# Optimization experiments

Hardware: AMD Instinct MI355X
Metric: run time of the kernel (lower is better)

## Reference

```python
import jax, jax.numpy as jnp
import numpy as np


def setup_inputs() -> dict:
    key = jax.random.key(0)
    ks = jax.random.split(key, 7)
    B, S, D, HD, m = 4, 8192, 2048, 128, 4
    s = 0.02
    return {
        "h": jax.random.normal(ks[0], (B, S, D), jnp.float32),
        "w_kv_a": jax.random.normal(ks[1], (D, HD), jnp.float32) * s,
        "w_kv_b": jax.random.normal(ks[2], (D, HD), jnp.float32) * s,
        "w_z_a": jax.random.normal(ks[3], (D, HD), jnp.float32) * s,
        "w_z_b": jax.random.normal(ks[4], (D, HD), jnp.float32) * s,
        "b_a": jax.random.normal(ks[5], (m, HD), jnp.float32) * s,
        "b_b": jax.random.normal(ks[6], (m, HD), jnp.float32) * s,
        "m": m,
    }


def reference(h, w_kv_a, w_kv_b, w_z_a, w_z_b, b_a, b_b, m):
    # h: [B, S, D]; weights stored as [D, head_dim] (torch Linear W^T)
    B, S, D = h.shape
    HD = w_kv_a.shape[1]
    n = S // m  # number of compressed blocks
    # Projections, reshaped into m-token blocks: [B, n, m, HD]
    c_a = (h @ w_kv_a).reshape(B, n, m, HD)
    c_b = (h @ w_kv_b).reshape(B, n, m, HD)
    z_a = (h @ w_z_a).reshape(B, n, m, HD)
    z_b = (h @ w_z_b).reshape(B, n, m, HD)

    def prev(x):  # previous block per position (block 0 has no predecessor)
        return jnp.concatenate([jnp.zeros_like(x[:, :1]), x[:, :-1]], axis=1)

    # Window of 2m logits per block: [prev-block b-branch, current-block a-branch]
    logits = jnp.concatenate([prev(z_b) + b_b, z_a + b_a], axis=2)  # [B, n, 2m, HD]
    # Block 0 only sees its own m tokens: mask out the (absent) previous half
    valid = jnp.concatenate(
        [jnp.broadcast_to((jnp.arange(n) > 0)[:, None], (n, m)),
         jnp.ones((n, m), bool)], axis=1)  # [n, 2m]
    neg = jnp.finfo(logits.dtype).min
    logits = jnp.where(valid[None, :, :, None], logits, neg)
    weights = jax.nn.softmax(logits, axis=2)  # softmax over the 2m window, per feature
    c_vals = jnp.concatenate([prev(c_b), c_a], axis=2)  # [B, n, 2m, HD]
    compressed = jnp.sum(weights * c_vals, axis=2)  # [B, n, HD]
    return compressed, compressed
```

## Files before the change

### kernel.cpp

```cpp
#include <hip/hip_runtime.h>

typedef unsigned short u16;
typedef unsigned int u32;
typedef float f32x4 __attribute__((ext_vector_type(4)));
typedef short bf16x8 __attribute__((ext_vector_type(8)));
typedef u16 u16x8 __attribute__((ext_vector_type(8)));

#define D_DIM 2048
#define HD_DIM 128
#define NCOLS 512
#define BM 128
#define HALO 16
#define MROWS 144
#define BK 32
#define KSTEPS 64
#define NTHREADS 512
#define OUT1 1048576

#define A_STRIDE 40
#define A_BYTES (MROWS * A_STRIDE * 2)
#define B_BYTES (NCOLS * BK * 2)
#define OFF_A0 0
#define OFF_A1 A_BYTES
#define OFF_B0 (2 * A_BYTES)
#define OFF_B1 (OFF_B0 + B_BYTES)
#define EPI_STRIDE 520
#define SMEM_BYTES (MROWS * EPI_STRIDE * 2)

__device__ __forceinline__ u16 f2bf(float f) {
  u32 u = __builtin_bit_cast(u32, f);
  u32 r = u + 0x7FFFu + ((u >> 16) & 1u);
  return (u16)(r >> 16);
}
__device__ __forceinline__ float bf2f(u16 v) {
  u32 u = ((u32)v) << 16;
  return __builtin_bit_cast(float, u);
}

__global__ __launch_bounds__(256) void wconv_kernel(
    const float* __restrict__ w0, const float* __restrict__ w1,
    const float* __restrict__ w2, const float* __restrict__ w3,
    u16* __restrict__ Wt) {
  __shared__ float tile[64][129];
  const int t = threadIdx.x;
  const int mat = blockIdx.x >> 5;
  const int k0 = (blockIdx.x & 31) << 6;
  const float* w = (mat == 0) ? w0 : (mat == 1) ? w1 : (mat == 2) ? w2 : w3;
#pragma unroll
  for (int i = 0; i < 32; ++i) {
    int idx = t + i * 256;
    int r = idx >> 7, c = idx & 127;
    tile[r][c] = w[(k0 + r) * HD_DIM + c];
  }
  __syncthreads();
#pragma unroll
  for (int i = 0; i < 32; ++i) {
    int idx = t + i * 256;
    int nl = idx >> 6, kk = idx & 63;
    Wt[(long)(mat * HD_DIM + nl) * D_DIM + k0 + kk] = f2bf(tile[kk][nl]);
  }
}

__global__ __launch_bounds__(NTHREADS, 2) void fused_kernel(
    const float* __restrict__ h, const u16* __restrict__ Wt,
    const float* __restrict__ ba, const float* __restrict__ bb,
    float* __restrict__ out) {
  __shared__ alignas(16) unsigned char smem[SMEM_BYTES];
  const int t = threadIdx.x;
  const int w = t >> 6;
  const int l = t & 63;
  const int r0 = blockIdx.x * BM;

  const int arow0 = t >> 2;
  const int aseg0 = t & 3;
  const int ag0 = r0 - HALO + arow0;
  const bool av0 = (ag0 >= 0);
  const float* asrc0 = h + (long)ag0 * D_DIM + aseg0 * 8;
  const int adst0 = arow0 * A_STRIDE + aseg0 * 8;

  const bool has2 = ((t & 7) == 0);
  const int q2 = 512 + (t >> 3);
  const int arow1 = q2 >> 2;
  const int aseg1 = q2 & 3;
  const float* asrc1 = h + (long)(r0 - HALO + arow1) * D_DIM + aseg1 * 8;
  const int adst1 = arow1 * A_STRIDE + aseg1 * 8;

  const int brow = t >> 2;
  const int bc = t & 3;
  const int bswz = bc ^ ((t >> 3) & 3);
  const u16* bsrc0 = Wt + (long)brow * D_DIM + bc * 8;
  const int bdst = brow * 32 + bswz * 8;

  const int aoff0 = (l & 15) * A_STRIDE + (l >> 4) * 8;
  const int swzr = (l >> 4) ^ ((l >> 1) & 3);
  const int boff0 = (w * 64 + (l & 15)) * 32 + swzr * 8;

  f32x4 acc[9][4];
#pragma unroll
  for (int mt = 0; mt < 9; ++mt)
#pragma unroll
    for (int nt = 0; nt < 4; ++nt) acc[mt][nt] = (f32x4){0.f, 0.f, 0.f, 0.f};

  float4 la0a, la0b, la1a, la1b;
  u16x8 bs0, bs1, bs2, bs3;

#define DO_LOADS(K0)                                          \
  {                                                           \
    const float4 z4 = make_float4(0.f, 0.f, 0.f, 0.f);        \
    la0a = av0 ? *(const float4*)(asrc0 + (K0)) : z4;         \
    la0b = av0 ? *(const float4*)(asrc0 + (K0) + 4) : z4;     \
    if (has2) {                                               \
      la1a = *(const float4*)(asrc1 + (K0));                  \
      la1b = *(const float4*)(asrc1 + (K0) + 4);              \
    }                                                         \
    bs0 = *(const u16x8*)(bsrc0 + (K0));                      \
    bs1 = *(const u16x8*)(bsrc0 + 128 * 2048 + (K0));         \
    bs2 = *(const u16x8*)(bsrc0 + 256 * 2048 + (K0));         \
    bs3 = *(const u16x8*)(bsrc0 + 384 * 2048 + (K0));         \
  }

#define DO_STORE(BUF)                                         \
  {                                                           \
    u16* Ab = (u16*)(smem + ((BUF) ? OFF_A1 : OFF_A0));       \
    u16* Bb = (u16*)(smem + ((BUF) ? OFF_B1 : OFF_B0));       \
    u16x8 pa;                                                 \
    pa[0] = f2bf(la0a.x); pa[1] = f2bf(la0a.y);               \
    pa[2] = f2bf(la0a.z); pa[3] = f2bf(la0a.w);               \
    pa[4] = f2bf(la0b.x); pa[5] = f2bf(la0b.y);               \
    pa[6] = f2bf(la0b.z); pa[7] = f2bf(la0b.w);               \
    *(u16x8*)(Ab + adst0) = pa;                               \
    if (has2) {                                               \
      u16x8 pb;                                               \
      pb[0] = f2bf(la1a.x); pb[1] = f2bf(la1a.y);             \
      pb[2] = f2bf(la1a.z); pb[3] = f2bf(la1a.w);             \
      pb[4] = f2bf(la1b.x); pb[5] = f2bf(la1b.y);             \
      pb[6] = f2bf(la1b.z); pb[7] = f2bf(la1b.w);             \
      *(u16x8*)(Ab + adst1) = pb;                             \
    }                                                         \
    *(u16x8*)(Bb + bdst) = bs0;                               \
    *(u16x8*)(Bb + 128 * 32 + bdst) = bs1;                    \
    *(u16x8*)(Bb + 256 * 32 + bdst) = bs2;                    \
    *(u16x8*)(Bb + 384 * 32 + bdst) = bs3;                    \
  }

  DO_LOADS(0)
  DO_STORE(0)
  __syncthreads();

  for (int step = 0; step < KSTEPS; ++step) {
    const int cur = step & 1;
    const bool more = (step + 1) < KSTEPS;
    if (more) DO_LOADS((step + 1) * BK)
    {
      const u16* Ab = (const u16*)(smem + (cur ? OFF_A1 : OFF_A0));
      const u16* Bb = (const u16*)(smem + (cur ? OFF_B1 : OFF_B0));
      bf16x8 bfr[4];
#pragma unroll
      for (int nt = 0; nt < 4; ++nt)
        bfr[nt] = *(const bf16x8*)(Bb + boff0 + nt * (16 * 32));
#pragma unroll
      for (int mt = 0; mt < 9; ++mt) {
        bf16x8 af = *(const bf16x8*)(Ab + aoff0 + mt * (16 * A_STRIDE));
#pragma unroll
        for (int nt = 0; nt < 4; ++nt)
          acc[mt][nt] = __builtin_amdgcn_mfma_f32_16x16x32_bf16(
              af, bfr[nt], acc[mt][nt], 0, 0, 0);
      }
    }
    if (more) DO_STORE(cur ^ 1)
    __syncthreads();
  }

  u16* E = (u16*)smem;
  {
    const int er = (l >> 4) * 4;
    const int ec = w * 64 + (l & 15);
#pragma unroll
    for (int mt = 0; mt < 9; ++mt)
#pragma unroll
      for (int nt = 0; nt < 4; ++nt)
#pragma unroll
        for (int j = 0; j < 4; ++j)
          E[(mt * 16 + er + j) * EPI_STRIDE + ec + nt * 16] =
              f2bf(acc[mt][nt][j]);
  }
  __syncthreads();

  {
    const int hd = t & 127;
    const int grp = t >> 7;
    const int b = r0 >> 13;
    const int sbase = r0 & 8191;
#pragma unroll
    for (int i = 0; i < 8; ++i) {
      const int nblk = grp * 8 + i;
      const int s_in = sbase + nblk * 4;
      const bool first = (s_in == 0);
      const int rc = HALO + nblk * 4;
      float la[4], lb[4], ca[4], cb[4];
#pragma unroll
      for (int j = 0; j < 4; ++j) {
        const u16* rowc = E + (rc + j) * EPI_STRIDE;
        const u16* rowp = E + (rc - 4 + j) * EPI_STRIDE;
        la[j] = bf2f(rowc[256 + hd]) + ba[j * 128 + hd];
        ca[j] = bf2f(rowc[hd]);
        lb[j] = first ? -3.0e38f
                      : (bf2f(rowp[384 + hd]) + bb[j * 128 + hd]);
        cb[j] = bf2f(rowp[128 + hd]);
      }
      float mx = la[0];
#pragma unroll
      for (int j = 1; j < 4; ++j) mx = fmaxf(mx, la[j]);
#pragma unroll
      for (int j = 0; j < 4; ++j) mx = fmaxf(mx, lb[j]);
      float num = 0.f, den = 0.f;
#pragma unroll
      for (int j = 0; j < 4; ++j) {
        float ea = __expf(la[j] - mx);
        num += ea * ca[j]; den += ea;
        float eb = __expf(lb[j] - mx);
        num += eb * cb[j]; den += eb;
      }
      const float res = num / den;
      const int o = ((b << 11) + (s_in >> 2)) * HD_DIM + hd;
      out[o] = res;
      out[o + OUT1] = res;
    }
  }
}

extern "C" void kernel_launch(void* const* d_in, const int* in_sizes, int n_in,
                              void* d_out, int out_size, void* d_ws,
                              size_t ws_size, hipStream_t stream) {
  (void)in_sizes; (void)n_in; (void)out_size; (void)ws_size;
  const float* h = (const float*)d_in[0];
  const float* w_kv_a = (const float*)d_in[1];
  const float* w_kv_b = (const float*)d_in[2];
  const float* w_z_a = (const float*)d_in[3];
  const float* w_z_b = (const float*)d_in[4];
  const float* b_a = (const float*)d_in[5];
  const float* b_b = (const float*)d_in[6];
  u16* Wt = (u16*)d_ws;
  float* out = (float*)d_out;
  wconv_kernel<<<128, 256, 0, stream>>>(w_kv_a, w_kv_b, w_z_a, w_z_b, Wt);
  fused_kernel<<<256, NTHREADS, 0, stream>>>(h, Wt, b_a, b_b, out);
}
```

Measured before the change: 496.5 us.

## Triple-buffer K loop with direct global-to-LDS weight loads and pre-swizzled weights

Pre-swizzles the bf16 weight matrix in the conversion kernel into per-K-step tiles in LDS order, so the main kernel can copy them straight from global memory into LDS with global_load_lds and skip the register round trip. The activation tile stays register-staged but is now prefetched two steps ahead, with a three-buffer LDS rotation, manual vmcnt waits and a single barrier per step. The goal is to hide global load latency behind MFMA work and cut VGPR and LDS-store instruction pressure. The cost is more complex hand-written waitcnt logic, a tighter LDS budget, and some correctness risk in the buffer indexing.

```diff
diff --git a/kernel.cpp b/kernel.cpp
--- a/kernel.cpp
+++ b/kernel.cpp
@@ -8,7 +8,6 @@
 
 #define D_DIM 2048
 #define HD_DIM 128
-#define NCOLS 512
 #define BM 128
 #define HALO 16
 #define MROWS 144
@@ -19,11 +18,8 @@
 
 #define A_STRIDE 40
 #define A_BYTES (MROWS * A_STRIDE * 2)
-#define B_BYTES (NCOLS * BK * 2)
-#define OFF_A0 0
-#define OFF_A1 A_BYTES
-#define OFF_B0 (2 * A_BYTES)
-#define OFF_B1 (OFF_B0 + B_BYTES)
+#define B_BYTES (512 * BK * 2)
+#define OFF_A (3 * B_BYTES)
 #define EPI_STRIDE 520
 #define SMEM_BYTES (MROWS * EPI_STRIDE * 2)
 
@@ -35,6 +31,12 @@
 __device__ __forceinline__ float bf2f(u16 v) {
   u32 u = ((u32)v) << 16;
   return __builtin_bit_cast(float, u);
+}
+
+__device__ __forceinline__ void gload_lds16(const u16* g, u16* l) {
+  __builtin_amdgcn_global_load_lds(
+      (const __attribute__((address_space(1))) unsigned int*)g,
+      (__attribute__((address_space(3))) unsigned int*)l, 16, 0, 0);
 }
 
 __global__ __launch_bounds__(256) void wconv_kernel(
@@ -57,7 +59,11 @@
   for (int i = 0; i < 32; ++i) {
     int idx = t + i * 256;
     int nl = idx >> 6, kk = idx & 63;
-    Wt[(long)(mat * HD_DIM + nl) * D_DIM + k0 + kk] = f2bf(tile[kk][nl]);
+    int n = mat * HD_DIM + nl;
+    int k = k0 + kk;
+    int stepi = k >> 5, kr = k & 31;
+    int pos = stepi * 16384 + n * 32 + (((kr >> 3) ^ ((n >> 1) & 3)) << 3) + (kr & 7);
+    Wt[pos] = f2bf(tile[kk][nl]);
   }
 }
 
@@ -71,25 +77,17 @@
   const int l = t & 63;
   const int r0 = blockIdx.x * BM;
 
-  const int arow0 = t >> 2;
-  const int aseg0 = t & 3;
+  const int arow0 = t >> 2, aseg0 = t & 3;
   const int ag0 = r0 - HALO + arow0;
   const bool av0 = (ag0 >= 0);
-  const float* asrc0 = h + (long)ag0 * D_DIM + aseg0 * 8;
+  const long ag0c = av0 ? (long)ag0 : 0l;
+  const float* asrc0 = h + ag0c * D_DIM + aseg0 * 8;
   const int adst0 = arow0 * A_STRIDE + aseg0 * 8;
-
   const bool has2 = ((t & 7) == 0);
-  const int q2 = 512 + (t >> 3);
-  const int arow1 = q2 >> 2;
-  const int aseg1 = q2 & 3;
+  const int arow1 = 128 + (t >> 5);
+  const int aseg1 = (t >> 3) & 3;
   const float* asrc1 = h + (long)(r0 - HALO + arow1) * D_DIM + aseg1 * 8;
   const int adst1 = arow1 * A_STRIDE + aseg1 * 8;
-
-  const int brow = t >> 2;
-  const int bc = t & 3;
-  const int bswz = bc ^ ((t >> 3) & 3);
-  const u16* bsrc0 = Wt + (long)brow * D_DIM + bc * 8;
-  const int bdst = brow * 32 + bswz * 8;
 
   const int aoff0 = (l & 15) * A_STRIDE + (l >> 4) * 8;
   const int swzr = (l >> 4) ^ ((l >> 1) & 3);
@@ -101,75 +99,108 @@
 #pragma unroll
     for (int nt = 0; nt < 4; ++nt) acc[mt][nt] = (f32x4){0.f, 0.f, 0.f, 0.f};
 
-  float4 la0a, la0b, la1a, la1b;
-  u16x8 bs0, bs1, bs2, bs3;
-
-#define DO_LOADS(K0)                                          \
-  {                                                           \
-    const float4 z4 = make_float4(0.f, 0.f, 0.f, 0.f);        \
-    la0a = av0 ? *(const float4*)(asrc0 + (K0)) : z4;         \
-    la0b = av0 ? *(const float4*)(asrc0 + (K0) + 4) : z4;     \
-    if (has2) {                                               \
-      la1a = *(const float4*)(asrc1 + (K0));                  \
-      la1b = *(const float4*)(asrc1 + (K0) + 4);              \
-    }                                                         \
-    bs0 = *(const u16x8*)(bsrc0 + (K0));                      \
-    bs1 = *(const u16x8*)(bsrc0 + 128 * 2048 + (K0));         \
-    bs2 = *(const u16x8*)(bsrc0 + 256 * 2048 + (K0));         \
-    bs3 = *(const u16x8*)(bsrc0 + 384 * 2048 + (K0));         \
-  }
-
-#define DO_STORE(BUF)                                         \
-  {                                                           \
-    u16* Ab = (u16*)(smem + ((BUF) ? OFF_A1 : OFF_A0));       \
-    u16* Bb = (u16*)(smem + ((BUF) ? OFF_B1 : OFF_B0));       \
-    u16x8 pa;                                                 \
-    pa[0] = f2bf(la0a.x); pa[1] = f2bf(la0a.y);               \
-    pa[2] = f2bf(la0a.z); pa[3] = f2bf(la0a.w);               \
-    pa[4] = f2bf(la0b.x); pa[5] = f2bf(la0b.y);               \
-    pa[6] = f2bf(la0b.z); pa[7] = f2bf(la0b.w);               \
-    *(u16x8*)(Ab + adst0) = pa;                               \
-    if (has2) {                                               \
-      u16x8 pb;                                               \
-      pb[0] = f2bf(la1a.x); pb[1] = f2bf(la1a.y);             \
-      pb[2] = f2bf(la1a.z); pb[3] = f2bf(la1a.w);             \
-      pb[4] = f2bf(la1b.x); pb[5] = f2bf(la1b.y);             \
-      pb[6] = f2bf(la1b.z); pb[7] = f2bf(la1b.w);             \
-      *(u16x8*)(Ab + adst1) = pb;                             \
-    }                                                         \
-    *(u16x8*)(Bb + bdst) = bs0;                               \
-    *(u16x8*)(Bb + 128 * 32 + bdst) = bs1;                    \
-    *(u16x8*)(Bb + 256 * 32 + bdst) = bs2;                    \
-    *(u16x8*)(Bb + 384 * 32 + bdst) = bs3;                    \
-  }
-
-  DO_LOADS(0)
-  DO_STORE(0)
+  float4 r0a, r0b, r0ha, r0hb, r1a, r1b, r1ha, r1hb;
+
+#define ISSUE_B(SI, BI)                                           \
+  {                                                               \
+    const u16* gsrc = Wt + (size_t)(SI) * 16384 + w * 2048 + l * 8; \
+    u16* lb = (u16*)(smem + (BI) * B_BYTES) + w * 2048;           \
+    gload_lds16(gsrc, lb);                                        \
+    gload_lds16(gsrc + 512, lb + 512);                            \
+    gload_lds16(gsrc + 1024, lb + 1024);                          \
+    gload_lds16(gsrc + 1536, lb + 1536);                          \
+  }
+
+#define ISSUE_A(SI, RA, RB, RHA, RHB)      \
+  {                                        \
+    const float* p0 = asrc0 + (SI) * BK;   \
+    RA = *(const float4*)(p0);             \
+    RB = *(const float4*)(p0 + 4);         \
+    if (has2) {                            \
+      const float* p1 = asrc1 + (SI) * BK; \
+      RHA = *(const float4*)(p1);          \
+      RHB = *(const float4*)(p1 + 4);      \
+    }                                      \
+  }
+
+#define WRITE_A(BI, RA, RB, RHA, RHB)                  \
+  {                                                    \
+    u16* Ab = (u16*)(smem + OFF_A + (BI) * A_BYTES);   \
+    u16x8 pa;                                          \
+    pa[0] = av0 ? f2bf(RA.x) : (u16)0;                 \
+    pa[1] = av0 ? f2bf(RA.y) : (u16)0;                 \
+    pa[2] = av0 ? f2bf(RA.z) : (u16)0;                 \
+    pa[3] = av0 ? f2bf(RA.w) : (u16)0;                 \
+    pa[4] = av0 ? f2bf(RB.x) : (u16)0;                 \
+    pa[5] = av0 ? f2bf(RB.y) : (u16)0;                 \
+    pa[6] = av0 ? f2bf(RB.z) : (u16)0;                 \
+    pa[7] = av0 ? f2bf(RB.w) : (u16)0;                 \
+    *(u16x8*)(Ab + adst0) = pa;                        \
+    if (has2) {                                        \
+      u16x8 pb;                                        \
+      pb[0] = f2bf(RHA.x); pb[1] = f2bf(RHA.y);        \
+      pb[2] = f2bf(RHA.z); pb[3] = f2bf(RHA.w);        \
+      pb[4] = f2bf(RHB.x); pb[5] = f2bf(RHB.y);        \
+      pb[6] = f2bf(RHB.z); pb[7] = f2bf(RHB.w);        \
+      *(u16x8*)(Ab + adst1) = pb;                      \
+    }                                                  \
+  }
+
+#define COMPUTE(BI)                                                         \
+  {                                                                         \
+    const u16* Ab = (const u16*)(smem + OFF_A + (BI) * A_BYTES);            \
+    const u16* Bb = (const u16*)(smem + (BI) * B_BYTES);                    \
+    bf16x8 bfr0 = *(const bf16x8*)(Bb + boff0);                             \
+    bf16x8 bfr1 = *(const bf16x8*)(Bb + boff0 + 512);                       \
+    bf16x8 bfr2 = *(const bf16x8*)(Bb + boff0 + 1024);                      \
+    bf16x8 bfr3 = *(const bf16x8*)(Bb + boff0 + 1536);                      \
+    _Pragma("unroll")                                                       \
+    for (int mt = 0; mt < 9; ++mt) {                                        \
+      bf16x8 af = *(const bf16x8*)(Ab + aoff0 + mt * (16 * A_STRIDE));      \
+      acc[mt][0] = __builtin_amdgcn_mfma_f32_16x16x32_bf16(af, bfr0, acc[mt][0], 0, 0, 0); \
+      acc[mt][1] = __builtin_amdgcn_mfma_f32_16x16x32_bf16(af, bfr1, acc[mt][1], 0, 0, 0); \
+      acc[mt][2] = __builtin_amdgcn_mfma_f32_16x16x32_bf16(af, bfr2, acc[mt][2], 0, 0, 0); \
+      acc[mt][3] = __builtin_amdgcn_mfma_f32_16x16x32_bf16(af, bfr3, acc[mt][3], 0, 0, 0); \
+    }                                                                       \
+  }
+
+#define VM_WAIT8() asm volatile("s_waitcnt vmcnt(8)" ::: "memory")
+#define VM_WAIT0() asm volatile("s_waitcnt vmcnt(0)" ::: "memory")
+#define SYNC_ITER()                                        \
+  {                                                        \
+    asm volatile("s_waitcnt lgkmcnt(0)" ::: "memory");     \
+    __builtin_amdgcn_s_barrier();                          \
+  }
+
+  ISSUE_B(0, 0)
+  ISSUE_A(0, r0a, r0b, r0ha, r0hb)
+  ISSUE_B(1, 1)
+  ISSUE_A(1, r1a, r1b, r1ha, r1hb)
+  VM_WAIT8();
+  WRITE_A(0, r0a, r0b, r0ha, r0hb)
+  SYNC_ITER();
+
+  for (int s = 0; s < KSTEPS - 2; s += 2) {
+    const int b0 = s % 3, b1 = (s + 1) % 3, b2 = (s + 2) % 3, b3 = (s + 3) % 3;
+    ISSUE_B(s + 2, b2)
+    ISSUE_A(s + 2, r0a, r0b, r0ha, r0hb)
+    VM_WAIT8();
+    WRITE_A(b1, r1a, r1b, r1ha, r1hb)
+    COMPUTE(b0)
+    SYNC_ITER();
+    ISSUE_B(s + 3, b3)
+    ISSUE_A(s + 3, r1a, r1b, r1ha, r1hb)
+    VM_WAIT8();
+    WRITE_A(b2, r0a, r0b, r0ha, r0hb)
+    COMPUTE(b1)
+    SYNC_ITER();
+  }
+  VM_WAIT0();
+  WRITE_A(0, r1a, r1b, r1ha, r1hb)
+  COMPUTE(2)
+  SYNC_ITER();
+  COMPUTE(0)
   __syncthreads();
-
-  for (int step = 0; step < KSTEPS; ++step) {
-    const int cur = step & 1;
-    const bool more = (step + 1) < KSTEPS;
-    if (more) DO_LOADS((step + 1) * BK)
-    {
-      const u16* Ab = (const u16*)(smem + (cur ? OFF_A1 : OFF_A0));
-      const u16* Bb = (const u16*)(smem + (cur ? OFF_B1 : OFF_B0));
-      bf16x8 bfr[4];
-#pragma unroll
-      for (int nt = 0; nt < 4; ++nt)
-        bfr[nt] = *(const bf16x8*)(Bb + boff0 + nt * (16 * 32));
-#pragma unroll
-      for (int mt = 0; mt < 9; ++mt) {
-        bf16x8 af = *(const bf16x8*)(Ab + aoff0 + mt * (16 * A_STRIDE));
-#pragma unroll
-        for (int nt = 0; nt < 4; ++nt)
-          acc[mt][nt] = __builtin_amdgcn_mfma_f32_16x16x32_bf16(
-              af, bfr[nt], acc[mt][nt], 0, 0, 0);
-      }
-    }
-    if (more) DO_STORE(cur ^ 1)
-    __syncthreads();
-  }
 
   u16* E = (u16*)smem;
   {
@@ -204,8 +235,7 @@
         const u16* rowp = E + (rc - 4 + j) * EPI_STRIDE;
         la[j] = bf2f(rowc[256 + hd]) + ba[j * 128 + hd];
         ca[j] = bf2f(rowc[hd]);
-        lb[j] = first ? -3.0e38f
-                      : (bf2f(rowp[384 + hd]) + bb[j * 128 + hd]);
+        lb[j] = first ? -3.0e38f : (bf2f(rowp[384 + hd]) + bb[j * 128 + hd]);
         cb[j] = bf2f(rowp[128 + hd]);
       }
       float mx = la[0];
```

Measured after the change: 421.5 us. 1.18x faster.
